# Kernel tuning notes

Hardware: AMD Instinct MI355X
Metric: run time of the kernel (lower is better)

## Reference

```python
import jax
import jax.numpy as jnp
import numpy as np

TAU = 0.2       # opt.tau
EPSILON = 1e-4  # opt.epsilon

B, C_IN, H, W = 64, 64, 64, 64
C_OUT, K = 128, 3


def setup_inputs() -> dict:
    key = jax.random.key(0)
    k1, k2, k3, k4 = jax.random.split(key, 4)
    x = jax.random.normal(k1, (B, C_IN, H, W), dtype=jnp.float32)
    # Conv2d default init scale ~ 1/sqrt(fan_in)
    fan_in = C_IN * K * K
    W_ff = jax.random.normal(k2, (C_OUT, C_IN, K, K), dtype=jnp.float32) / np.sqrt(fan_in)
    # W_rec starts at zeros in __init__, but after training postprocess makes it
    # non-negative with zero diagonal; use a small such matrix to exercise the loop.
    r = jax.random.uniform(k3, (C_OUT, C_OUT), dtype=jnp.float32) * 0.01
    r = r * (1.0 - jnp.eye(C_OUT, dtype=jnp.float32))
    W_rec = r[:, :, None, None]
    threshold = 0.1 * jax.random.normal(k4, (C_OUT,), dtype=jnp.float32)
    return {"input": x, "W_ff": W_ff, "W_rec": W_rec, "threshold": threshold}


def reference(input, W_ff, W_rec, threshold):
    # u_0 = W_ff * input  (VALID 3x3 conv, no bias)
    u0 = jax.lax.conv_general_dilated(
        input, W_ff, window_strides=(1, 1), padding="VALID",
        dimension_numbers=("NCHW", "OIHW", "NCHW"))  # [B, C_OUT, H-K+1, W-K+1]
    a0 = jax.lax.stop_gradient(jax.nn.relu(u0))
    thr = threshold[None, :, None, None]
    Wr = W_rec[:, :, 0, 0]  # 1x1 conv == channel mixing matrix [C_OUT, C_OUT]

    def cond_fn(carry):
        u, u_old, a, i = carry
        ratio = jnp.linalg.norm(u - u_old) / jnp.linalg.norm(u)
        # first iteration must always run (u == 0 gives NaN ratio; NaN>=eps is False)
        return jnp.logical_or(i == 0, ratio >= EPSILON)

    def body_fn(carry):
        u, u_old, a, i = carry
        lateral = jnp.einsum("oc,bchw->bohw", Wr, a)
        u_new = (1.0 - TAU) * u + TAU * (u0 - lateral)
        a_new = jax.lax.stop_gradient(jax.nn.relu(u_new - thr))
        return (u_new, u, a_new, i + 1)

    z = jnp.zeros_like(u0)
    carry = (z, z, a0, jnp.int32(0))
    _, _, a_final, _ = jax.lax.while_loop(cond_fn, body_fn, carry)
    return jax.lax.stop_gradient(a_final)
```

## Files before the change

### kernel.cpp

```cpp
#include <hip/hip_runtime.h>
#include <hip/hip_bf16.h>

typedef __bf16 bf16x8 __attribute__((ext_vector_type(8)));
typedef __bf16 bf16x4 __attribute__((ext_vector_type(4)));
typedef float  f32x4  __attribute__((ext_vector_type(4)));
typedef float  f32x16 __attribute__((ext_vector_type(16)));

#define B_    64
#define CIN   64
#define HIN   64
#define WIN   64
#define COUT  128
#define HO    62
#define WO    62
#define NPIX  (B_*HO*WO)
#define NITER 10

#define PIN_A(x) asm volatile("" : "+a"(x))
#define PIN_V(x) asm volatile("" : "+v"(x))

__global__ void prep_w_kernel(const float* __restrict__ wff,
                              const float* __restrict__ wrec,
                              __bf16* __restrict__ wt,
                              __bf16* __restrict__ wrp) {
  int i = blockIdx.x * 256 + threadIdx.x;
  const int NW = 9 * COUT * CIN;
  if (i < NW) {
    int tap = i / (COUT * CIN);
    int rem = i % (COUT * CIN);
    int o = rem >> 6;
    int c = rem & 63;
    int kh = tap / 3, kw = tap % 3;
    wt[i] = (__bf16)wff[((o * CIN + c) * 3 + kh) * 3 + kw];
  } else {
    int j = i - NW;
    if (j < 32 * 64 * 8) {
      int e    = j & 7;
      int lane = (j >> 3) & 63;
      int fk   = j >> 9;
      int mt = fk >> 2, kt = fk & 3;
      int m    = mt * 16 + (lane & 15);
      int quad = lane >> 4;
      int ch   = kt * 16 + ((e >> 2) << 6) + quad * 4 + (e & 3);
      wrp[j] = (__bf16)(-wrec[m * COUT + ch]);
    }
  }
}

__global__ void prep_x_kernel(const float* __restrict__ x,
                              __bf16* __restrict__ xh) {
  __shared__ float t[64][65];
  int tid = threadIdx.x;
  int b = blockIdx.x >> 6;
  int h = blockIdx.x & 63;
#pragma unroll
  for (int it = 0; it < 16; ++it) {
    int c = it * 4 + (tid >> 6);
    int w = tid & 63;
    t[c][w] = x[(((size_t)(b * 64 + c)) * 64 + h) * 64 + w];
  }
  __syncthreads();
  size_t rowbase = (size_t)blockIdx.x * 4096;
#pragma unroll
  for (int it = 0; it < 16; ++it) {
    int j = it * 256 + tid;
    int c8  = j & 7;
    int w   = (j >> 3) & 63;
    int grp = j >> 9;
    xh[rowbase + j] = (__bf16)t[grp * 8 + c8][w];
  }
}

__global__ __launch_bounds__(256, 2) void conv_kernel(
    const __bf16* __restrict__ xh, const __bf16* __restrict__ wt,
    float* __restrict__ u0) {
  __shared__ __align__(16) __bf16 xs[6 * 8 * 64 * 8];
  int tid  = threadIdx.x;
  int lane = tid & 63;
  int wv   = tid >> 6;
  int hg   = blockIdx.x;
  int b    = blockIdx.y;

#pragma unroll
  for (int i = 0; i < 12; ++i) {
    int chunk = wv * 12 + i;
    int row = chunk >> 3;
    int part = chunk & 7;
    int row_src = hg * 4 + row;
    if (row_src > 63) row_src = 63;
    const __bf16* g = xh + ((size_t)(b * 64 + row_src)) * 4096 + part * 512 + lane * 8;
    __bf16* l = xs + chunk * 512;
    __builtin_amdgcn_global_load_lds(
        (const __attribute__((address_space(1))) void*)g,
        (__attribute__((address_space(3))) void*)l, 16, 0, 0);
  }

  int m31 = lane & 31;
  int khalf = lane >> 5;
  bf16x8 Wf[36];
#pragma unroll
  for (int tap = 0; tap < 9; ++tap)
#pragma unroll
    for (int k4 = 0; k4 < 4; ++k4)
      Wf[tap * 4 + k4] = *(const bf16x8*)
          &wt[((size_t)tap * COUT + wv * 32 + m31) * CIN + k4 * 16 + khalf * 8];
#pragma unroll
  for (int i = 0; i < 36; ++i) PIN_A(Wf[i]);

  __syncthreads();

#pragma unroll 1
  for (int nt = 0; nt < 8; ++nt) {
    int px = nt * 32 + m31;
    int r = (px >= 62) + (px >= 124) + (px >= 186) + (px >= 248);
    if (r > 3) r = 3;
    int wcol = px - r * 62;
    if (wcol > 61) wcol = 61;
    int orow = hg * 4 + r;
    bool valid = (px < 248) && (orow < 62);
    const char* lbase = (const char*)xs + (((r * 8 + khalf) * 64 + wcol) << 4);

    f32x16 acc0, acc1;
#pragma unroll
    for (int q = 0; q < 16; ++q) { acc0[q] = 0.f; acc1[q] = 0.f; }

#pragma unroll
    for (int tap = 0; tap < 9; ++tap) {
      int kh = tap / 3, kw = tap % 3;
#pragma unroll
      for (int k4 = 0; k4 < 4; ++k4) {
        bf16x8 Bf = *(const bf16x8*)(lbase + kh * 8192 + k4 * 2048 + kw * 16);
        int idx = tap * 4 + k4;
        if (idx & 1) acc1 = __builtin_amdgcn_mfma_f32_32x32x16_bf16(Wf[idx], Bf, acc1, 0, 0, 0);
        else         acc0 = __builtin_amdgcn_mfma_f32_32x32x16_bf16(Wf[idx], Bf, acc0, 0, 0, 0);
      }
    }
    if (valid) {
      size_t pix = ((size_t)b * HO + orow) * WO + wcol;
      float* up = u0 + pix * COUT + wv * 32 + khalf * 4;
#pragma unroll
      for (int g4 = 0; g4 < 4; ++g4) {
        f32x4 v;
#pragma unroll
        for (int q = 0; q < 4; ++q) v[q] = acc0[g4 * 4 + q] + acc1[g4 * 4 + q];
        *(f32x4*)&up[g4 * 8] = v;
      }
    }
  }
}

__global__ __launch_bounds__(256, 3) void iterate_kernel(
    const float* __restrict__ u0, const __bf16* __restrict__ wrp,
    const float* __restrict__ thr, float* __restrict__ out) {
  __shared__ __align__(16) __bf16 wrl[32 * 64 * 8];
  int tid = threadIdx.x;
  int lane = tid & 63, wv = tid >> 6;
  int l15 = lane & 15, quad = lane >> 4;
  size_t p = (size_t)blockIdx.x * 64 + wv * 16 + l15;
  int pb = (int)(p / (HO * WO));
  int pr = (int)(p % (HO * WO));

#pragma unroll
  for (int i = 0; i < 8; ++i) {
    const __bf16* g = wrp + (size_t)(i * 256 + tid) * 8;
    __bf16* l = wrl + (i * 256 + tid) * 8;
    __builtin_amdgcn_global_load_lds(
        (const __attribute__((address_space(1))) void*)g,
        (__attribute__((address_space(3))) void*)l, 16, 0, 0);
  }

  f32x4 u0f[8];
#pragma unroll
  for (int mt = 0; mt < 8; ++mt) {
    f32x4 u = *(const f32x4*)&u0[p * COUT + mt * 16 + quad * 4];
    f32x4 t = *(const f32x4*)&thr[mt * 16 + quad * 4];
    u0f[mt] = u - t;
  }
#pragma unroll
  for (int mt = 0; mt < 8; ++mt) PIN_A(u0f[mt]);

  f32x4 acc[8];
#pragma unroll
  for (int mt = 0; mt < 8; ++mt) { acc[mt] = u0f[mt]; PIN_A(acc[mt]); }

  __syncthreads();

  const __bf16* afrag = &wrl[(size_t)lane * 8];

  bf16x8 Bf[4];
#pragma unroll 1
  for (int it = 0; it < NITER; ++it) {
#pragma unroll
    for (int kt = 0; kt < 4; ++kt) {
      bf16x8 v;
#pragma unroll
      for (int e = 0; e < 4; ++e) v[e]     = (__bf16)fmaxf(acc[kt][e],     0.f);
#pragma unroll
      for (int e = 0; e < 4; ++e) v[e + 4] = (__bf16)fmaxf(acc[kt + 4][e], 0.f);
      Bf[kt] = v;
    }
#pragma unroll
    for (int mt = 0; mt < 8; ++mt) {
      f32x4 a = u0f[mt];
#pragma unroll
      for (int kt = 0; kt < 4; ++kt) {
        bf16x8 Af = *(const bf16x8*)(afrag + (size_t)(mt * 4 + kt) * 512);
        a = __builtin_amdgcn_mfma_f32_16x16x32_bf16(Af, Bf[kt], a, 0, 0, 0);
      }
      acc[mt] = a;
      PIN_A(acc[mt]);
    }
  }
  {
#pragma unroll
    for (int kt = 0; kt < 4; ++kt) {
      bf16x8 v;
#pragma unroll
      for (int e = 0; e < 4; ++e) v[e]     = (__bf16)fmaxf(acc[kt][e],     0.f);
#pragma unroll
      for (int e = 0; e < 4; ++e) v[e + 4] = (__bf16)fmaxf(acc[kt + 4][e], 0.f);
      Bf[kt] = v;
    }
#pragma unroll
    for (int mt = 0; mt < 8; ++mt) {
      f32x4 a = u0f[mt];
#pragma unroll
      for (int kt = 0; kt < 4; ++kt) {
        bf16x8 Af = *(const bf16x8*)(afrag + (size_t)(mt * 4 + kt) * 512);
        a = __builtin_amdgcn_mfma_f32_16x16x32_bf16(Af, Bf[kt], a, 0, 0, 0);
      }
#pragma unroll
      for (int r = 0; r < 4; ++r) {
        int ch = mt * 16 + quad * 4 + r;
        out[((size_t)pb * COUT + ch) * (HO * WO) + pr] = fmaxf(a[r], 0.f);
      }
    }
  }
}

extern "C" void kernel_launch(void* const* d_in, const int* in_sizes, int n_in,
                              void* d_out, int out_size, void* d_ws, size_t ws_size,
                              hipStream_t stream) {
  const float* x    = (const float*)d_in[0];
  const float* wff  = (const float*)d_in[1];
  const float* wrec = (const float*)d_in[2];
  const float* thr  = (const float*)d_in[3];
  float* out = (float*)d_out;

  char* ws = (char*)d_ws;
  size_t off = 0;
  float*  u0 = (float*)(ws + off);  off += (size_t)NPIX * COUT * 4;
  __bf16* xh = (__bf16*)(ws + off); off += (size_t)B_ * HIN * WIN * CIN * 2;
  __bf16* wt = (__bf16*)(ws + off); off += (size_t)9 * COUT * CIN * 2;
  __bf16* wrp = (__bf16*)(ws + off); off += (size_t)32 * 64 * 8 * 2;

  prep_w_kernel<<<352, 256, 0, stream>>>(wff, wrec, wt, wrp);
  prep_x_kernel<<<B_ * HIN, 256, 0, stream>>>(x, xh);
  conv_kernel<<<dim3(16, B_), 256, 0, stream>>>(xh, wt, u0);
  iterate_kernel<<<NPIX / 64, 256, 0, stream>>>(u0, wrp, thr, out);
}
```

Before: 326.7 us.

## Keep part of recurrent weights in registers and pair output tiles in iterate kernel

The iterate kernel now keeps the first 12 recurrent-weight A fragments in registers and stages only the remaining 20 in LDS, which cuts LDS traffic and footprint. The M-tile loop is reorganised to compute tile pairs (kt2, kt2+4) together, so each pair is ReLU-packed into the next B fragment as soon as it is done, and the packing uses explicit v_cvt_pk_bf16_f32. This removes the separate full-accumulator array and per-iteration conversion pass. In exchange it adds register pressure, which may threaten the 3-block occupancy target.

```diff
diff --git a/kernel.cpp b/kernel.cpp
--- a/kernel.cpp
+++ b/kernel.cpp
@@ -15,9 +15,23 @@
 #define WO    62
 #define NPIX  (B_*HO*WO)
 #define NITER 10
+#define NPERS 3
 
 #define PIN_A(x) asm volatile("" : "+a"(x))
 #define PIN_V(x) asm volatile("" : "+v"(x))
+
+__device__ __forceinline__ bf16x8 relu_pack_pair(f32x4 a0, f32x4 a1) {
+  union { unsigned int w[4]; bf16x8 v; } u;
+  float l0 = fmaxf(a0[0], 0.f), l1 = fmaxf(a0[1], 0.f);
+  float l2 = fmaxf(a0[2], 0.f), l3 = fmaxf(a0[3], 0.f);
+  float h0 = fmaxf(a1[0], 0.f), h1 = fmaxf(a1[1], 0.f);
+  float h2 = fmaxf(a1[2], 0.f), h3 = fmaxf(a1[3], 0.f);
+  asm("v_cvt_pk_bf16_f32 %0, %1, %2" : "=v"(u.w[0]) : "v"(l0), "v"(l1));
+  asm("v_cvt_pk_bf16_f32 %0, %1, %2" : "=v"(u.w[1]) : "v"(l2), "v"(l3));
+  asm("v_cvt_pk_bf16_f32 %0, %1, %2" : "=v"(u.w[2]) : "v"(h0), "v"(h1));
+  asm("v_cvt_pk_bf16_f32 %0, %1, %2" : "=v"(u.w[3]) : "v"(h2), "v"(h3));
+  return u.v;
+}
 
 __global__ void prep_w_kernel(const float* __restrict__ wff,
                               const float* __restrict__ wrec,
@@ -152,7 +166,7 @@
 __global__ __launch_bounds__(256, 3) void iterate_kernel(
     const float* __restrict__ u0, const __bf16* __restrict__ wrp,
     const float* __restrict__ thr, float* __restrict__ out) {
-  __shared__ __align__(16) __bf16 wrl[32 * 64 * 8];
+  __shared__ __align__(16) __bf16 wrl[20 * 64 * 8];
   int tid = threadIdx.x;
   int lane = tid & 63, wv = tid >> 6;
   int l15 = lane & 15, quad = lane >> 4;
@@ -161,14 +175,21 @@
   int pr = (int)(p % (HO * WO));
 
 #pragma unroll
-  for (int i = 0; i < 8; ++i) {
-    const __bf16* g = wrp + (size_t)(i * 256 + tid) * 8;
+  for (int i = 0; i < 5; ++i) {
+    const __bf16* g = wrp + (size_t)12 * 512 + (size_t)(i * 256 + tid) * 8;
     __bf16* l = wrl + (i * 256 + tid) * 8;
     __builtin_amdgcn_global_load_lds(
         (const __attribute__((address_space(1))) void*)g,
         (__attribute__((address_space(3))) void*)l, 16, 0, 0);
   }
 
+  bf16x8 Afp[12];
+#pragma unroll
+  for (int j = 0; j < 12; ++j)
+    Afp[j] = *(const bf16x8*)&wrp[((size_t)j * 64 + lane) * 8];
+#pragma unroll
+  for (int j = 0; j < 12; ++j) PIN_A(Afp[j]);
+
   f32x4 u0f[8];
 #pragma unroll
   for (int mt = 0; mt < 8; ++mt) {
@@ -179,61 +200,59 @@
 #pragma unroll
   for (int mt = 0; mt < 8; ++mt) PIN_A(u0f[mt]);
 
-  f32x4 acc[8];
-#pragma unroll
-  for (int mt = 0; mt < 8; ++mt) { acc[mt] = u0f[mt]; PIN_A(acc[mt]); }
+  bf16x8 Bc[4];
+#pragma unroll
+  for (int kt = 0; kt < 4; ++kt) Bc[kt] = relu_pack_pair(u0f[kt], u0f[kt + 4]);
 
   __syncthreads();
 
   const __bf16* afrag = &wrl[(size_t)lane * 8];
 
-  bf16x8 Bf[4];
 #pragma unroll 1
   for (int it = 0; it < NITER; ++it) {
+    bf16x8 Bn[4];
+#pragma unroll
+    for (int kt2 = 0; kt2 < 4; ++kt2) {
+      f32x4 a0 = u0f[kt2];
+      f32x4 a1 = u0f[kt2 + 4];
+#pragma unroll
+      for (int kt = 0; kt < 4; ++kt) {
+        bf16x8 A1 = *(const bf16x8*)(afrag + (size_t)((kt2 + 4) * 4 + kt - 12) * 512);
+        if (kt2 < NPERS) {
+          a0 = __builtin_amdgcn_mfma_f32_16x16x32_bf16(Afp[kt2 * 4 + kt], Bc[kt], a0, 0, 0, 0);
+        } else {
+          bf16x8 A0 = *(const bf16x8*)(afrag + (size_t)(kt2 * 4 + kt - 12) * 512);
+          a0 = __builtin_amdgcn_mfma_f32_16x16x32_bf16(A0, Bc[kt], a0, 0, 0, 0);
+        }
+        a1 = __builtin_amdgcn_mfma_f32_16x16x32_bf16(A1, Bc[kt], a1, 0, 0, 0);
+      }
+      Bn[kt2] = relu_pack_pair(a0, a1);
+    }
+#pragma unroll
+    for (int kt = 0; kt < 4; ++kt) Bc[kt] = Bn[kt];
+  }
+
+#pragma unroll
+  for (int kt2 = 0; kt2 < 4; ++kt2) {
+    f32x4 a0 = u0f[kt2];
+    f32x4 a1 = u0f[kt2 + 4];
 #pragma unroll
     for (int kt = 0; kt < 4; ++kt) {
-      bf16x8 v;
-#pragma unroll
-      for (int e = 0; e < 4; ++e) v[e]     = (__bf16)fmaxf(acc[kt][e],     0.f);
-#pragma unroll
-      for (int e = 0; e < 4; ++e) v[e + 4] = (__bf16)fmaxf(acc[kt + 4][e], 0.f);
-      Bf[kt] = v;
-    }
-#pragma unroll
-    for (int mt = 0; mt < 8; ++mt) {
-      f32x4 a = u0f[mt];
-#pragma unroll
-      for (int kt = 0; kt < 4; ++kt) {
-        bf16x8 Af = *(const bf16x8*)(afrag + (size_t)(mt * 4 + kt) * 512);
-        a = __builtin_amdgcn_mfma_f32_16x16x32_bf16(Af, Bf[kt], a, 0, 0, 0);
-      }
-      acc[mt] = a;
-      PIN_A(acc[mt]);
-    }
-  }
-  {
-#pragma unroll
-    for (int kt = 0; kt < 4; ++kt) {
-      bf16x8 v;
-#pragma unroll
-      for (int e = 0; e < 4; ++e) v[e]     = (__bf16)fmaxf(acc[kt][e],     0.f);
-#pragma unroll
-      for (int e = 0; e < 4; ++e) v[e + 4] = (__bf16)fmaxf(acc[kt + 4][e], 0.f);
-      Bf[kt] = v;
-    }
-#pragma unroll
-    for (int mt = 0; mt < 8; ++mt) {
-      f32x4 a = u0f[mt];
-#pragma unroll
-      for (int kt = 0; kt < 4; ++kt) {
-        bf16x8 Af = *(const bf16x8*)(afrag + (size_t)(mt * 4 + kt) * 512);
-        a = __builtin_amdgcn_mfma_f32_16x16x32_bf16(Af, Bf[kt], a, 0, 0, 0);
-      }
-#pragma unroll
-      for (int r = 0; r < 4; ++r) {
-        int ch = mt * 16 + quad * 4 + r;
-        out[((size_t)pb * COUT + ch) * (HO * WO) + pr] = fmaxf(a[r], 0.f);
-      }
+      bf16x8 A1 = *(const bf16x8*)(afrag + (size_t)((kt2 + 4) * 4 + kt - 12) * 512);
+      if (kt2 < NPERS) {
+        a0 = __builtin_amdgcn_mfma_f32_16x16x32_bf16(Afp[kt2 * 4 + kt], Bc[kt], a0, 0, 0, 0);
+      } else {
+        bf16x8 A0 = *(const bf16x8*)(afrag + (size_t)(kt2 * 4 + kt - 12) * 512);
+        a0 = __builtin_amdgcn_mfma_f32_16x16x32_bf16(A0, Bc[kt], a0, 0, 0, 0);
+      }
+      a1 = __builtin_amdgcn_mfma_f32_16x16x32_bf16(A1, Bc[kt], a1, 0, 0, 0);
+    }
+#pragma unroll
+    for (int r = 0; r < 4; ++r) {
+      int ch0 = kt2 * 16 + quad * 4 + r;
+      int ch1 = (kt2 + 4) * 16 + quad * 4 + r;
+      out[((size_t)pb * COUT + ch0) * (HO * WO) + pr] = fmaxf(a0[r], 0.f);
+      out[((size_t)pb * COUT + ch1) * (HO * WO) + pr] = fmaxf(a1[r], 0.f);
     }
   }
 }
```

Result: slower. 374.3 us (+14.6%).
